# Kernel tuning notes

Measured on AMD Instinct MI355X. Metric: run time of the kernel, lower is better.

Reference implementation:

```python
import jax, jax.numpy as jnp
import numpy as np

M_MARGIN = 0.2   # Config.MARGIN_ARCFACE
S_SCALE = 16.0   # Config.SCALE_ARCFACE
EPS = 1e-7
L2_EPS = 1e-12   # torch F.normalize eps

N, D, C = 8192, 512, 32000


def _l2_normalize(x, axis=-1):
    # matches torch F.normalize: x / max(||x||, eps)
    norm = jnp.sqrt(jnp.sum(x * x, axis=axis, keepdims=True))
    return x / jnp.maximum(norm, L2_EPS)


def setup_inputs() -> dict:
    key = jax.random.key(0)
    k1, k2, k3 = jax.random.split(key, 3)
    prev_output = jax.random.normal(k1, (N, D), dtype=jnp.float32)
    # xavier_uniform_ init for weight [C, D]
    limit = float(np.sqrt(6.0 / (C + D)))
    weight = jax.random.uniform(k2, (C, D), dtype=jnp.float32, minval=-limit, maxval=limit)
    labels = jax.random.randint(k3, (N,), 0, C, dtype=jnp.int64)
    return {"prev_output": prev_output, "weight": weight, "labels": labels}


def reference(prev_output, weight, labels):
    x = _l2_normalize(prev_output)          # [N, D]
    w = _l2_normalize(weight)               # [C, D]
    cosine = jnp.einsum('nd,cd->nc', x, w)  # [N, C]
    theta = jnp.arccos(jnp.clip(cosine, -1.0 + EPS, 1.0 - EPS))
    margin_logits = jnp.cos(theta + M_MARGIN)
    one_hot = (jnp.arange(cosine.shape[1])[None, :] == labels[:, None])
    logits = jnp.where(one_hot, margin_logits, cosine) * S_SCALE
    logp = jax.nn.log_softmax(logits, axis=-1)
    nll = -jnp.take_along_axis(logp, labels[:, None], axis=1)[:, 0]
    return jnp.mean(nll)
```

## Files before the change

### kernel.cpp

```cpp
#include <hip/hip_runtime.h>


typedef __attribute__((ext_vector_type(4))) float f32x4;
typedef __attribute__((ext_vector_type(16))) float f32x16;
typedef __attribute__((ext_vector_type(4))) int i32x4;
typedef __attribute__((ext_vector_type(8))) int i32x8;

constexpr int N = 8192, D = 512, C = 32000;
constexpr int BM = 256;
constexpr int NSPLIT = 16;
constexpr int CPS = C / NSPLIT;
constexpr int GCH = 63;
constexpr int KS8 = 8;
constexpr int XBLK = N / 4;
constexpr float SCL = 16.0f;
constexpr float LOG2E = 1.4426950408889634f;
constexpr float S2 = SCL * LOG2E;
constexpr float COSM = 0.98006657784124163f;
constexpr float SINM = 0.19866933079506122f;
constexpr float EPSC = 1e-7f;
constexpr float EM16 = 1.12535174719259114e-07f;
constexpr float FEC = 1064871712.0f;

__device__ __forceinline__ unsigned enc_fp4(float v, float inv) {
  unsigned s = (__float_as_uint(v) >> 31) << 3;
  float m = fabsf(v) * inv;
  float r = m < 2.0f ? 2.0f * m : (m < 4.0f ? m + 2.0f : fmaf(m, 0.5f, 4.0f));
  unsigned q = (unsigned)(r + 0.5f);
  return s | (q > 7u ? 7u : q);
}

__device__ __forceinline__ void block_scale(float amax, unsigned& eB, float& inv) {
  unsigned u = __float_as_uint(amax * (1.0f / 6.0f));
  eB = (u >> 23) & 255u;
  if (u & 0x7fffffu) eB += 1u;
  if (eB < 1u) eB = 1u;
  if (eB > 254u) eB = 254u;
  inv = __uint_as_float((254u - eB) << 23);
}

__device__ __forceinline__ i32x8 up8(i32x4 v) {
  return __builtin_shufflevector(v, v, 0, 1, 2, 3, -1, -1, -1, -1);
}

__global__ void k_prep(const float* __restrict__ x, const float* __restrict__ w,
                       const int* __restrict__ labels,
                       unsigned* __restrict__ xn4, unsigned char* __restrict__ xsc,
                       unsigned char* __restrict__ wt4, unsigned char* __restrict__ wsc,
                       float* __restrict__ coslab, float* __restrict__ outz) {
  __shared__ unsigned lbuf[2048];
  __shared__ unsigned char sbuf[512];
  const int tid = threadIdx.x, wv = tid >> 6, L = tid & 63;
  if (blockIdx.x == 0 && tid == 0) *outz = 0.0f;

  if (blockIdx.x < XBLK) {
    int r = (blockIdx.x << 2) + wv;
    const float* row = x + (size_t)r * D;
    float f[8];
    *(f32x4*)&f[0] = *(const f32x4*)(row + L * 8);
    *(f32x4*)&f[4] = *(const f32x4*)(row + L * 8 + 4);
    float ss = 0.f;
    #pragma unroll
    for (int i = 0; i < 8; ++i) ss += f[i] * f[i];
    const float* wr = w + (size_t)labels[r] * D;
    float p[8];
    *(f32x4*)&p[0] = *(const f32x4*)(wr + L * 8);
    *(f32x4*)&p[4] = *(const f32x4*)(wr + L * 8 + 4);
    float ww = 0.f, xw = 0.f;
    #pragma unroll
    for (int i = 0; i < 8; ++i) { ww += p[i] * p[i]; xw += f[i] * p[i]; }
    #pragma unroll
    for (int m = 1; m <= 32; m <<= 1) {
      ss += __shfl_xor(ss, m, 64);
      ww += __shfl_xor(ww, m, 64);
      xw += __shfl_xor(xw, m, 64);
    }
    if (L == 0)
      coslab[r] = xw / (fmaxf(sqrtf(ss), 1e-12f) * fmaxf(sqrtf(ww), 1e-12f));
    float sc = S2 / fmaxf(sqrtf(ss), 1e-12f);
    float v[8], am = 0.f;
    #pragma unroll
    for (int i = 0; i < 8; ++i) { v[i] = f[i] * sc; am = fmaxf(am, fabsf(v[i])); }
    am = fmaxf(am, __shfl_xor(am, 1, 64));
    am = fmaxf(am, __shfl_xor(am, 2, 64));
    unsigned eB; float inv;
    block_scale(am, eB, inv);
    unsigned pk = 0;
    #pragma unroll
    for (int j = 0; j < 8; ++j) pk |= enc_fp4(v[j], inv) << (4 * j);
    xn4[(size_t)r * 64 + L] = pk;
    if ((L & 3) == 0) {
      int kb = L >> 2;
      xsc[(size_t)r * 16 + (kb & 1) * 8 + (kb >> 1)] = (unsigned char)eB;
    }
    return;
  }

  const int gidx = blockIdx.x - XBLK;
  const int sp = gidx / GCH, within = gidx % GCH;
  #pragma unroll
  for (int t = 0; t < 8; ++t) {
    int rl = t * 4 + wv;
    int colin = within * 32 + rl;
    bool valid = colin < CPS;
    unsigned pk = 0;
    unsigned eB = 1u;
    if (valid) {
      const float* row = w + ((size_t)sp * CPS + colin) * D;
      float f[8];
      *(f32x4*)&f[0] = *(const f32x4*)(row + L * 8);
      *(f32x4*)&f[4] = *(const f32x4*)(row + L * 8 + 4);
      float ss = 0.f;
      #pragma unroll
      for (int i = 0; i < 8; ++i) ss += f[i] * f[i];
      #pragma unroll
      for (int m = 1; m <= 32; m <<= 1) ss += __shfl_xor(ss, m, 64);
      float sc = 1.0f / fmaxf(sqrtf(ss), 1e-12f);
      float v[8], am = 0.f;
      #pragma unroll
      for (int i = 0; i < 8; ++i) { v[i] = f[i] * sc; am = fmaxf(am, fabsf(v[i])); }
      am = fmaxf(am, __shfl_xor(am, 1, 64));
      am = fmaxf(am, __shfl_xor(am, 2, 64));
      float inv;
      block_scale(am, eB, inv);
      #pragma unroll
      for (int j = 0; j < 8; ++j) pk |= enc_fp4(v[j], inv) << (4 * j);
    }
    lbuf[(L >> 3) * 256 + (((L >> 2) & 1) * 32 + rl) * 4 + (L & 3)] = pk;
    if ((L & 3) == 0) {
      int kb = L >> 2;
      sbuf[rl * 16 + (kb & 1) * 8 + (kb >> 1)] = (unsigned char)eB;
    }
  }
  __syncthreads();
  uint4* dst = (uint4*)(wt4 + (size_t)gidx * 8192);
  #pragma unroll
  for (int i = 0; i < 2; ++i) dst[i * 256 + tid] = ((const uint4*)lbuf)[i * 256 + tid];
  if (tid < 128)
    ((unsigned*)(wsc + (size_t)gidx * 512))[tid] = ((const unsigned*)sbuf)[tid];
}

#define KS_STEP(KSL)                                                          \
    __builtin_amdgcn_s_setprio(1);                                            \
    acc0 = __builtin_amdgcn_mfma_scale_f32_32x32x64_f8f6f4(                   \
        up8(af4[0][KSL]), up8(b4[KSL]), (KSL) == 0 ? fzero : acc0,            \
        4, 4, (KSL) & 3, ((KSL) >> 2) ? ascB0 : ascA0,                        \
              (KSL) & 3, ((KSL) >> 2) ? bscB : bscA);                         \
    acc1 = __builtin_amdgcn_mfma_scale_f32_32x32x64_f8f6f4(                   \
        up8(af4[1][KSL]), up8(b4[KSL]), (KSL) == 0 ? fzero : acc1,            \
        4, 4, (KSL) & 3, ((KSL) >> 2) ? ascB1 : ascA1,                        \
              (KSL) & 3, ((KSL) >> 2) ? bscB : bscA);                         \
    __builtin_amdgcn_s_setprio(0);                                            \
    b4[KSL] = *(const i32x4*)(pnx + (KSL) * 1024);

#define CHUNK_STEP                                                            \
  {                                                                           \
    int nscA = *(const int*)gscn;                                             \
    int nscB = *(const int*)(gscn + 4);                                       \
    KS_STEP(0)                                                                \
    KS_STEP(1)                                                                \
    KS_STEP(2)                                                                \
    KS_STEP(3)                                                                \
    KS_STEP(4)                                                                \
    KS_STEP(5)                                                                \
    KS_STEP(6)                                                                \
    KS_STEP(7)                                                                \
    _Pragma("unroll")                                                         \
    for (int i = 0; i < 16; ++i) {                                            \
      accS0[i] += __uint_as_float((unsigned)fmaf(acc0[i], 8388608.0f, FEC));  \
      accS1[i] += __uint_as_float((unsigned)fmaf(acc1[i], 8388608.0f, FEC));  \
    }                                                                         \
    bscA = nscA; bscB = nscB;                                                 \
    pnx += 8192; gscn += 512;                                                 \
  }

__global__ __launch_bounds__(256, 2) void k_fused(
    const unsigned char* __restrict__ xn4, const unsigned char* __restrict__ xsc,
    const unsigned char* __restrict__ wt4, const unsigned char* __restrict__ wsc,
    float* __restrict__ pS) {
  const int tid = threadIdx.x;
  const int wv = tid >> 6, lane = tid & 63;
  const int h = lane >> 5, c = lane & 31;
  const int bid = blockIdx.x;
  const int logical = (bid & 7) * 64 + (bid >> 3);
  const int sp = logical >> 5;
  const int rb = logical & 31;
  const int row0 = rb * BM + wv * 64;

  i32x4 af4[2][KS8];
  int ascA0, ascB0, ascA1, ascB1;
  {
    const unsigned char* x0 = xn4 + (size_t)(row0 + c) * 256 + h * 16;
    const unsigned char* x1 = xn4 + (size_t)(row0 + 32 + c) * 256 + h * 16;
    #pragma unroll
    for (int ks = 0; ks < KS8; ++ks) {
      af4[0][ks] = *(const i32x4*)(x0 + ks * 32);
      af4[1][ks] = *(const i32x4*)(x1 + ks * 32);
    }
    ascA0 = *(const int*)(xsc + (size_t)(row0 + c) * 16 + h * 8);
    ascB0 = *(const int*)(xsc + (size_t)(row0 + c) * 16 + h * 8 + 4);
    ascA1 = *(const int*)(xsc + (size_t)(row0 + 32 + c) * 16 + h * 8);
    ascB1 = *(const int*)(xsc + (size_t)(row0 + 32 + c) * 16 + h * 8 + 4);
  }

  float accS0[16], accS1[16];
  #pragma unroll
  for (int i = 0; i < 16; ++i) { accS0[i] = 0.0f; accS1[i] = 0.0f; }

  const f32x16 fzero = (f32x16)0.0f;

  const unsigned char* gb = wt4 + (size_t)(sp * GCH) * 8192 + lane * 16;
  const unsigned char* gscn = wsc + (size_t)(sp * GCH) * 512 + c * 16 + h * 8;

  i32x4 b4[KS8];
  #pragma unroll
  for (int ks = 0; ks < KS8; ++ks) b4[ks] = *(const i32x4*)(gb + ks * 1024);
  int bscA = *(const int*)gscn;
  int bscB = *(const int*)(gscn + 4);
  const unsigned char* pnx = gb + 8192;
  gscn += 512;

  f32x16 acc0, acc1;

  for (int ch = 0; ch < GCH; ++ch) {
    CHUNK_STEP
  }

  #pragma unroll
  for (int i = 0; i < 16; ++i) {
    float S0 = accS0[i], S1 = accS1[i];
    #pragma unroll
    for (int m = 1; m <= 16; m <<= 1) {
      S0 += __shfl_xor(S0, m, 64);
      S1 += __shfl_xor(S1, m, 64);
    }
    accS0[i] = S0; accS1[i] = S1;
  }
  if (c == 0) {
    #pragma unroll
    for (int i = 0; i < 16; ++i) {
      int rl = (i & 3) + 8 * (i >> 2) + 4 * h;
      pS[(size_t)sp * N + row0 + rl] = accS0[i];
      pS[(size_t)sp * N + row0 + 32 + rl] = accS1[i];
    }
  }
}
#undef CHUNK_STEP
#undef KS_STEP

__global__ void k_merge(const float* __restrict__ pS, const float* __restrict__ coslab,
                        float* __restrict__ out) {
  int row = blockIdx.x * 256 + threadIdx.x;
  float S = 0.0f;
  #pragma unroll
  for (int s = 0; s < NSPLIT; ++s) S += pS[(size_t)s * N + row];
  S -= 256.0f * __uint_as_float((unsigned)FEC);
  float cl = coslab[row];
  float zp = SCL * cl;
  float ccl = fminf(fmaxf(cl, -1.0f + EPSC), 1.0f - EPSC);
  float zm = SCL * (ccl * COSM - sqrtf(1.0f - ccl * ccl) * SINM);
  float denom = S * EM16 - __expf(zp - SCL) + __expf(zm - SCL);
  float nll = SCL + logf(denom) - zm;
  #pragma unroll
  for (int m = 1; m <= 32; m <<= 1) nll += __shfl_xor(nll, m, 64);
  __shared__ float part[4];
  if ((threadIdx.x & 63) == 0) part[threadIdx.x >> 6] = nll;
  __syncthreads();
  if (threadIdx.x == 0)
    atomicAdd(out, (part[0] + part[1] + part[2] + part[3]) * (1.0f / N));
}

extern "C" void kernel_launch(void* const* d_in, const int* in_sizes, int n_in,
                              void* d_out, int out_size, void* d_ws, size_t ws_size,
                              hipStream_t stream) {
  const float* x = (const float*)d_in[0];
  const float* w = (const float*)d_in[1];
  const int* labels = (const int*)d_in[2];
  float* out = (float*)d_out;

  unsigned char* xn4 = (unsigned char*)d_ws;
  unsigned char* xsc = xn4 + (size_t)N * 256;
  unsigned char* wt4 = xsc + (size_t)N * 16;
  unsigned char* wsc = wt4 + (size_t)NSPLIT * GCH * 8192;
  float* pS = (float*)(wsc + (size_t)NSPLIT * GCH * 512);
  float* coslab = pS + (size_t)NSPLIT * N;

  hipLaunchKernelGGL(k_prep, dim3(XBLK + NSPLIT * GCH), dim3(256), 0, stream,
                     x, w, labels, (unsigned*)xn4, xsc, wt4, wsc, coslab, out);
  hipLaunchKernelGGL(k_fused, dim3(32 * NSPLIT), dim3(256), 0, stream,
                     xn4, xsc, wt4, wsc, pS);
  hipLaunchKernelGGL(k_merge, dim3(N / 256), dim3(256), 0, stream, pS, coslab, out);
}
```

Baseline: 97.30 us.

## Stage weight tiles in double-buffered LDS via direct global-to-LDS loads, halve row tile

The kernel now loads weight chunks straight from global memory into double-buffered LDS with global_load_lds, and each wave reads its B operands from LDS. Before, every wave loaded the whole chunk from global memory into registers. The row tile drops from 256 to 128, so each wave covers 32 rows with one accumulator. The grid doubles and occupancy is set to 4 blocks per CU. This is meant to cut redundant global and L2 traffic for weights and raise occupancy, at the cost of a barrier per chunk and less MFMA work per loaded B tile.

```diff
diff --git a/kernel.cpp b/kernel.cpp
--- a/kernel.cpp
+++ b/kernel.cpp
@@ -7,7 +7,7 @@
 typedef __attribute__((ext_vector_type(8))) int i32x8;
 
 constexpr int N = 8192, D = 512, C = 32000;
-constexpr int BM = 256;
+constexpr int BM = 128;
 constexpr int NSPLIT = 16;
 constexpr int CPS = C / NSPLIT;
 constexpr int GCH = 63;
@@ -43,6 +43,12 @@
   return __builtin_shufflevector(v, v, 0, 1, 2, 3, -1, -1, -1, -1);
 }
 
+__device__ __forceinline__ void gload_lds16(const void* g, void* l) {
+  __builtin_amdgcn_global_load_lds(
+      (const __attribute__((address_space(1))) void*)g,
+      (__attribute__((address_space(3))) void*)l, 16, 0, 0);
+}
+
 __global__ void k_prep(const float* __restrict__ x, const float* __restrict__ w,
                        const int* __restrict__ labels,
                        unsigned* __restrict__ xn4, unsigned char* __restrict__ xsc,
@@ -141,111 +147,98 @@
 }
 
 #define KS_STEP(KSL)                                                          \
-    __builtin_amdgcn_s_setprio(1);                                            \
-    acc0 = __builtin_amdgcn_mfma_scale_f32_32x32x64_f8f6f4(                   \
-        up8(af4[0][KSL]), up8(b4[KSL]), (KSL) == 0 ? fzero : acc0,            \
-        4, 4, (KSL) & 3, ((KSL) >> 2) ? ascB0 : ascA0,                        \
-              (KSL) & 3, ((KSL) >> 2) ? bscB : bscA);                         \
-    acc1 = __builtin_amdgcn_mfma_scale_f32_32x32x64_f8f6f4(                   \
-        up8(af4[1][KSL]), up8(b4[KSL]), (KSL) == 0 ? fzero : acc1,            \
-        4, 4, (KSL) & 3, ((KSL) >> 2) ? ascB1 : ascA1,                        \
-              (KSL) & 3, ((KSL) >> 2) ? bscB : bscA);                         \
-    __builtin_amdgcn_s_setprio(0);                                            \
-    b4[KSL] = *(const i32x4*)(pnx + (KSL) * 1024);
-
-#define CHUNK_STEP                                                            \
-  {                                                                           \
-    int nscA = *(const int*)gscn;                                             \
-    int nscB = *(const int*)(gscn + 4);                                       \
-    KS_STEP(0)                                                                \
-    KS_STEP(1)                                                                \
-    KS_STEP(2)                                                                \
-    KS_STEP(3)                                                                \
-    KS_STEP(4)                                                                \
-    KS_STEP(5)                                                                \
-    KS_STEP(6)                                                                \
-    KS_STEP(7)                                                                \
-    _Pragma("unroll")                                                         \
-    for (int i = 0; i < 16; ++i) {                                            \
-      accS0[i] += __uint_as_float((unsigned)fmaf(acc0[i], 8388608.0f, FEC));  \
-      accS1[i] += __uint_as_float((unsigned)fmaf(acc1[i], 8388608.0f, FEC));  \
-    }                                                                         \
-    bscA = nscA; bscB = nscB;                                                 \
-    pnx += 8192; gscn += 512;                                                 \
-  }
-
-__global__ __launch_bounds__(256, 2) void k_fused(
+    {                                                                         \
+      i32x4 b = *(const i32x4*)(lbase + (KSL) * 1024);                        \
+      __builtin_amdgcn_s_setprio(1);                                          \
+      acc = __builtin_amdgcn_mfma_scale_f32_32x32x64_f8f6f4(                  \
+          up8(af4[KSL]), up8(b), (KSL) == 0 ? fzero : acc,                    \
+          4, 4, (KSL) & 3, ((KSL) >> 2) ? ascB : ascA,                        \
+                (KSL) & 3, ((KSL) >> 2) ? bscB : bscA);                       \
+      __builtin_amdgcn_s_setprio(0);                                          \
+    }
+
+__global__ __launch_bounds__(256, 4) void k_fused(
     const unsigned char* __restrict__ xn4, const unsigned char* __restrict__ xsc,
     const unsigned char* __restrict__ wt4, const unsigned char* __restrict__ wsc,
     float* __restrict__ pS) {
+  __shared__ __align__(16) unsigned char wbuf[2][8192];
   const int tid = threadIdx.x;
   const int wv = tid >> 6, lane = tid & 63;
   const int h = lane >> 5, c = lane & 31;
   const int bid = blockIdx.x;
-  const int logical = (bid & 7) * 64 + (bid >> 3);
-  const int sp = logical >> 5;
-  const int rb = logical & 31;
-  const int row0 = rb * BM + wv * 64;
-
-  i32x4 af4[2][KS8];
-  int ascA0, ascB0, ascA1, ascB1;
+  const int logical = (bid & 7) * 128 + (bid >> 3);
+  const int sp = logical >> 6;
+  const int rb = logical & 63;
+  const int row0 = rb * BM + wv * 32;
+
+  i32x4 af4[KS8];
+  int ascA, ascB;
   {
-    const unsigned char* x0 = xn4 + (size_t)(row0 + c) * 256 + h * 16;
-    const unsigned char* x1 = xn4 + (size_t)(row0 + 32 + c) * 256 + h * 16;
-    #pragma unroll
-    for (int ks = 0; ks < KS8; ++ks) {
-      af4[0][ks] = *(const i32x4*)(x0 + ks * 32);
-      af4[1][ks] = *(const i32x4*)(x1 + ks * 32);
-    }
-    ascA0 = *(const int*)(xsc + (size_t)(row0 + c) * 16 + h * 8);
-    ascB0 = *(const int*)(xsc + (size_t)(row0 + c) * 16 + h * 8 + 4);
-    ascA1 = *(const int*)(xsc + (size_t)(row0 + 32 + c) * 16 + h * 8);
-    ascB1 = *(const int*)(xsc + (size_t)(row0 + 32 + c) * 16 + h * 8 + 4);
-  }
-
-  float accS0[16], accS1[16];
-  #pragma unroll
-  for (int i = 0; i < 16; ++i) { accS0[i] = 0.0f; accS1[i] = 0.0f; }
+    const unsigned char* xr = xn4 + (size_t)(row0 + c) * 256 + h * 16;
+    #pragma unroll
+    for (int ks = 0; ks < KS8; ++ks) af4[ks] = *(const i32x4*)(xr + ks * 32);
+    ascA = *(const int*)(xsc + (size_t)(row0 + c) * 16 + h * 8);
+    ascB = *(const int*)(xsc + (size_t)(row0 + c) * 16 + h * 8 + 4);
+  }
+
+  float accS[16];
+  #pragma unroll
+  for (int i = 0; i < 16; ++i) accS[i] = 0.0f;
 
   const f32x16 fzero = (f32x16)0.0f;
 
-  const unsigned char* gb = wt4 + (size_t)(sp * GCH) * 8192 + lane * 16;
+  const unsigned char* gstage = wt4 + (size_t)(sp * GCH) * 8192
+                              + wv * 2048 + lane * 16;
   const unsigned char* gscn = wsc + (size_t)(sp * GCH) * 512 + c * 16 + h * 8;
-
-  i32x4 b4[KS8];
-  #pragma unroll
-  for (int ks = 0; ks < KS8; ++ks) b4[ks] = *(const i32x4*)(gb + ks * 1024);
+  const unsigned char* lbase = &wbuf[0][0] + lane * 16;
+
+  gload_lds16(gstage, &wbuf[0][0] + wv * 2048);
+  gload_lds16(gstage + 1024, &wbuf[0][0] + wv * 2048 + 1024);
   int bscA = *(const int*)gscn;
   int bscB = *(const int*)(gscn + 4);
-  const unsigned char* pnx = gb + 8192;
   gscn += 512;
-
-  f32x16 acc0, acc1;
-
+  __syncthreads();
+
+  f32x16 acc;
+  int cur = 0;
   for (int ch = 0; ch < GCH; ++ch) {
-    CHUNK_STEP
+    if (ch + 1 < GCH) {
+      const unsigned char* gs = gstage + (size_t)(ch + 1) * 8192;
+      gload_lds16(gs, &wbuf[cur ^ 1][0] + wv * 2048);
+      gload_lds16(gs + 1024, &wbuf[cur ^ 1][0] + wv * 2048 + 1024);
+    }
+    int nscA = *(const int*)gscn;
+    int nscB = *(const int*)(gscn + 4);
+
+    KS_STEP(0) KS_STEP(1) KS_STEP(2) KS_STEP(3)
+    KS_STEP(4) KS_STEP(5) KS_STEP(6) KS_STEP(7)
+
+    #pragma unroll
+    for (int i = 0; i < 16; ++i)
+      accS[i] += __uint_as_float((unsigned)fmaf(acc[i], 8388608.0f, FEC));
+
+    bscA = nscA; bscB = nscB;
+    gscn += 512;
+    __syncthreads();
+    cur ^= 1;
+    lbase = &wbuf[cur][0] + lane * 16;
   }
 
   #pragma unroll
   for (int i = 0; i < 16; ++i) {
-    float S0 = accS0[i], S1 = accS1[i];
-    #pragma unroll
-    for (int m = 1; m <= 16; m <<= 1) {
-      S0 += __shfl_xor(S0, m, 64);
-      S1 += __shfl_xor(S1, m, 64);
-    }
-    accS0[i] = S0; accS1[i] = S1;
+    float S = accS[i];
+    #pragma unroll
+    for (int m = 1; m <= 16; m <<= 1) S += __shfl_xor(S, m, 64);
+    accS[i] = S;
   }
   if (c == 0) {
     #pragma unroll
     for (int i = 0; i < 16; ++i) {
       int rl = (i & 3) + 8 * (i >> 2) + 4 * h;
-      pS[(size_t)sp * N + row0 + rl] = accS0[i];
-      pS[(size_t)sp * N + row0 + 32 + rl] = accS1[i];
-    }
-  }
-}
-#undef CHUNK_STEP
+      pS[(size_t)sp * N + row0 + rl] = accS[i];
+    }
+  }
+}
 #undef KS_STEP
 
 __global__ void k_merge(const float* __restrict__ pS, const float* __restrict__ coslab,
@@ -287,7 +280,7 @@
 
   hipLaunchKernelGGL(k_prep, dim3(XBLK + NSPLIT * GCH), dim3(256), 0, stream,
                      x, w, labels, (unsigned*)xn4, xsc, wt4, wsc, coslab, out);
-  hipLaunchKernelGGL(k_fused, dim3(32 * NSPLIT), dim3(256), 0, stream,
+  hipLaunchKernelGGL(k_fused, dim3(64 * NSPLIT), dim3(256), 0, stream,
                      xn4, xsc, wt4, wsc, pS);
   hipLaunchKernelGGL(k_merge, dim3(N / 256), dim3(256), 0, stream, pS, coslab, out);
 }
```

Result: slower. 104.3 us (+7.2%).

## Double-buffer MFMA accumulators to overlap exp epilogue with next chunk

Applied to the files above, without the earlier changes.

Uses two alternating pairs of MFMA accumulators so that the exp-sum epilogue of the previous weight chunk runs between the MFMA instructions of the current chunk. The loop is unrolled by two with a peeled first chunk and a final epilogue after the loop. This aims to hide the VALU exp and accumulate work behind matrix-core execution instead of serialising it after each chunk. It costs 32 more accumulator registers per thread, which could cause spills or scheduling pressure under the 2-blocks-per-SIMD launch bound.

```diff
diff --git a/kernel.cpp b/kernel.cpp
--- a/kernel.cpp
+++ b/kernel.cpp
@@ -140,36 +140,42 @@
     ((unsigned*)(wsc + (size_t)gidx * 512))[tid] = ((const unsigned*)sbuf)[tid];
 }
 
-#define KS_STEP(KSL)                                                          \
+#define KS_STEP(KSL, A0, A1, P0, P1, DOEXP)                                   \
     __builtin_amdgcn_s_setprio(1);                                            \
-    acc0 = __builtin_amdgcn_mfma_scale_f32_32x32x64_f8f6f4(                   \
-        up8(af4[0][KSL]), up8(b4[KSL]), (KSL) == 0 ? fzero : acc0,            \
+    A0 = __builtin_amdgcn_mfma_scale_f32_32x32x64_f8f6f4(                     \
+        up8(af4[0][KSL]), up8(b4[KSL]), (KSL) == 0 ? fzero : A0,              \
         4, 4, (KSL) & 3, ((KSL) >> 2) ? ascB0 : ascA0,                        \
               (KSL) & 3, ((KSL) >> 2) ? bscB : bscA);                         \
-    acc1 = __builtin_amdgcn_mfma_scale_f32_32x32x64_f8f6f4(                   \
-        up8(af4[1][KSL]), up8(b4[KSL]), (KSL) == 0 ? fzero : acc1,            \
+    A1 = __builtin_amdgcn_mfma_scale_f32_32x32x64_f8f6f4(                     \
+        up8(af4[1][KSL]), up8(b4[KSL]), (KSL) == 0 ? fzero : A1,              \
         4, 4, (KSL) & 3, ((KSL) >> 2) ? ascB1 : ascA1,                        \
               (KSL) & 3, ((KSL) >> 2) ? bscB : bscA);                         \
     __builtin_amdgcn_s_setprio(0);                                            \
+    if (DOEXP) {                                                              \
+      _Pragma("unroll")                                                       \
+      for (int r = 0; r < 4; ++r) {                                           \
+        if ((KSL) < 4)                                                        \
+          accS0[((KSL) & 3) * 4 + r] += __uint_as_float(                      \
+              (unsigned)fmaf(P0[((KSL) & 3) * 4 + r], 8388608.0f, FEC));      \
+        else                                                                  \
+          accS1[((KSL) & 3) * 4 + r] += __uint_as_float(                      \
+              (unsigned)fmaf(P1[((KSL) & 3) * 4 + r], 8388608.0f, FEC));      \
+      }                                                                       \
+    }                                                                         \
     b4[KSL] = *(const i32x4*)(pnx + (KSL) * 1024);
 
-#define CHUNK_STEP                                                            \
+#define CHUNK_STEP(A0, A1, P0, P1, DOEXP)                                     \
   {                                                                           \
     int nscA = *(const int*)gscn;                                             \
     int nscB = *(const int*)(gscn + 4);                                       \
-    KS_STEP(0)                                                                \
-    KS_STEP(1)                                                                \
-    KS_STEP(2)                                                                \
-    KS_STEP(3)                                                                \
-    KS_STEP(4)                                                                \
-    KS_STEP(5)                                                                \
-    KS_STEP(6)                                                                \
-    KS_STEP(7)                                                                \
-    _Pragma("unroll")                                                         \
-    for (int i = 0; i < 16; ++i) {                                            \
-      accS0[i] += __uint_as_float((unsigned)fmaf(acc0[i], 8388608.0f, FEC));  \
-      accS1[i] += __uint_as_float((unsigned)fmaf(acc1[i], 8388608.0f, FEC));  \
-    }                                                                         \
+    KS_STEP(0, A0, A1, P0, P1, DOEXP)                                         \
+    KS_STEP(1, A0, A1, P0, P1, DOEXP)                                         \
+    KS_STEP(2, A0, A1, P0, P1, DOEXP)                                         \
+    KS_STEP(3, A0, A1, P0, P1, DOEXP)                                         \
+    KS_STEP(4, A0, A1, P0, P1, DOEXP)                                         \
+    KS_STEP(5, A0, A1, P0, P1, DOEXP)                                         \
+    KS_STEP(6, A0, A1, P0, P1, DOEXP)                                         \
+    KS_STEP(7, A0, A1, P0, P1, DOEXP)                                         \
     bscA = nscA; bscB = nscB;                                                 \
     pnx += 8192; gscn += 512;                                                 \
   }
@@ -220,10 +226,18 @@
   const unsigned char* pnx = gb + 8192;
   gscn += 512;
 
-  f32x16 acc0, acc1;
-
-  for (int ch = 0; ch < GCH; ++ch) {
-    CHUNK_STEP
+  f32x16 accP0, accP1, accQ0, accQ1;
+
+  CHUNK_STEP(accP0, accP1, accQ0, accQ1, false)
+
+  for (int ch = 1; ch + 1 < GCH; ch += 2) {
+    CHUNK_STEP(accQ0, accQ1, accP0, accP1, true)
+    CHUNK_STEP(accP0, accP1, accQ0, accQ1, true)
+  }
+  #pragma unroll
+  for (int i = 0; i < 16; ++i) {
+    accS0[i] += __uint_as_float((unsigned)fmaf(accP0[i], 8388608.0f, FEC));
+    accS1[i] += __uint_as_float((unsigned)fmaf(accP1[i], 8388608.0f, FEC));
   }
 
   #pragma unroll
```

Result: slower. 139.6 us (+43.5%).

## Interleave exp-sum epilogue with MFMA chain via software-pipelined accumulators

Applied to the files above, without the earlier changes.

The MFMA sequence is reordered so that all eight acc0 K-steps run first, followed by all eight acc1 K-steps. The bit-trick exp accumulation for one accumulator is spread across the MFMAs of the other: acc0's sums are folded in during the acc1 chain, and acc1's sums are deferred to the next chunk's acc0 chain, with the first chunk peeled and an epilogue added. The aim is to hide the VALU exp/accumulate work behind matrix-core latency instead of running it serially after each chunk. The cost is a longer dependency distance per accumulator, higher register pressure, and reliance on the compiler keeping the interleaved order.

```diff
diff --git a/kernel.cpp b/kernel.cpp
--- a/kernel.cpp
+++ b/kernel.cpp
@@ -140,36 +140,41 @@
     ((unsigned*)(wsc + (size_t)gidx * 512))[tid] = ((const unsigned*)sbuf)[tid];
 }
 
-#define KS_STEP(KSL)                                                          \
+#define KS_T0(KSL, DOEXP)                                                     \
     __builtin_amdgcn_s_setprio(1);                                            \
     acc0 = __builtin_amdgcn_mfma_scale_f32_32x32x64_f8f6f4(                   \
         up8(af4[0][KSL]), up8(b4[KSL]), (KSL) == 0 ? fzero : acc0,            \
         4, 4, (KSL) & 3, ((KSL) >> 2) ? ascB0 : ascA0,                        \
               (KSL) & 3, ((KSL) >> 2) ? bscB : bscA);                         \
+    __builtin_amdgcn_s_setprio(0);                                            \
+    if (DOEXP) {                                                              \
+      accS1[2 * (KSL)] += __uint_as_float(                                    \
+          (unsigned)fmaf(acc1[2 * (KSL)], 8388608.0f, FEC));                  \
+      accS1[2 * (KSL) + 1] += __uint_as_float(                                \
+          (unsigned)fmaf(acc1[2 * (KSL) + 1], 8388608.0f, FEC));              \
+    }
+
+#define KS_T1(KSL)                                                            \
+    __builtin_amdgcn_s_setprio(1);                                            \
     acc1 = __builtin_amdgcn_mfma_scale_f32_32x32x64_f8f6f4(                   \
         up8(af4[1][KSL]), up8(b4[KSL]), (KSL) == 0 ? fzero : acc1,            \
         4, 4, (KSL) & 3, ((KSL) >> 2) ? ascB1 : ascA1,                        \
               (KSL) & 3, ((KSL) >> 2) ? bscB : bscA);                         \
     __builtin_amdgcn_s_setprio(0);                                            \
+    accS0[2 * (KSL)] += __uint_as_float(                                      \
+        (unsigned)fmaf(acc0[2 * (KSL)], 8388608.0f, FEC));                    \
+    accS0[2 * (KSL) + 1] += __uint_as_float(                                  \
+        (unsigned)fmaf(acc0[2 * (KSL) + 1], 8388608.0f, FEC));                \
     b4[KSL] = *(const i32x4*)(pnx + (KSL) * 1024);
 
-#define CHUNK_STEP                                                            \
+#define CHUNK_STEP(DOEXP)                                                     \
   {                                                                           \
     int nscA = *(const int*)gscn;                                             \
     int nscB = *(const int*)(gscn + 4);                                       \
-    KS_STEP(0)                                                                \
-    KS_STEP(1)                                                                \
-    KS_STEP(2)                                                                \
-    KS_STEP(3)                                                                \
-    KS_STEP(4)                                                                \
-    KS_STEP(5)                                                                \
-    KS_STEP(6)                                                                \
-    KS_STEP(7)                                                                \
-    _Pragma("unroll")                                                         \
-    for (int i = 0; i < 16; ++i) {                                            \
-      accS0[i] += __uint_as_float((unsigned)fmaf(acc0[i], 8388608.0f, FEC));  \
-      accS1[i] += __uint_as_float((unsigned)fmaf(acc1[i], 8388608.0f, FEC));  \
-    }                                                                         \
+    KS_T0(0, DOEXP) KS_T0(1, DOEXP) KS_T0(2, DOEXP) KS_T0(3, DOEXP)           \
+    KS_T0(4, DOEXP) KS_T0(5, DOEXP) KS_T0(6, DOEXP) KS_T0(7, DOEXP)           \
+    KS_T1(0) KS_T1(1) KS_T1(2) KS_T1(3)                                       \
+    KS_T1(4) KS_T1(5) KS_T1(6) KS_T1(7)                                       \
     bscA = nscA; bscB = nscB;                                                 \
     pnx += 8192; gscn += 512;                                                 \
   }
@@ -222,9 +227,13 @@
 
   f32x16 acc0, acc1;
 
-  for (int ch = 0; ch < GCH; ++ch) {
-    CHUNK_STEP
-  }
+  CHUNK_STEP(false)
+  for (int ch = 1; ch < GCH; ++ch) {
+    CHUNK_STEP(true)
+  }
+  #pragma unroll
+  for (int i = 0; i < 16; ++i)
+    accS1[i] += __uint_as_float((unsigned)fmaf(acc1[i], 8388608.0f, FEC));
 
   #pragma unroll
   for (int i = 0; i < 16; ++i) {
@@ -246,7 +255,8 @@
   }
 }
 #undef CHUNK_STEP
-#undef KS_STEP
+#undef KS_T0
+#undef KS_T1
 
 __global__ void k_merge(const float* __restrict__ pS, const float* __restrict__ coslab,
                         float* __restrict__ out) {
```

After: 97.81 us. About the same (+0.5%).
